# Optimization experiments

Measured on AMD Instinct MI355X. Metric: run time of the kernel, lower is better.

The kernel has to match this reference:

```python
import jax, jax.numpy as jnp
import numpy as np

NEG_INF = jnp.float32(-1e30)
EPS = 1e-7  # keras.backend.ctc_batch_cost epsilon


def ctc_batch_cost(y_true, y_pred):
    """Faithful CTC loss (keras ctc_batch_cost semantics): y_pred are
    probabilities [B,T,C], blank = C-1, full input/label lengths.
    Returns per-example negative log likelihood [B,1]."""
    B, T, C = y_pred.shape
    L = y_true.shape[1]
    S = 2 * L + 1  # extended label length (blanks interleaved)
    blank = C - 1

    log_probs = jnp.log(y_pred + EPS)  # [B,T,C]

    # Extended label sequence: blank, l0, blank, l1, ..., blank  -> [B,S]
    ext = jnp.full((B, S), blank, dtype=y_true.dtype)
    ext = ext.at[:, 1::2].set(y_true)

    # Skip transition allowed at s if ext[s] != blank and ext[s] != ext[s-2]
    skip = jnp.concatenate(
        [jnp.zeros((B, 2), dtype=bool),
         (ext[:, 2:] != blank) & (ext[:, 2:] != ext[:, :-2])], axis=1)  # [B,S]

    # Gather log-probs of extended labels per timestep: [T,B,S]
    lp_ext = jnp.take_along_axis(log_probs, ext[:, None, :], axis=2)  # [B,T,S]
    lp_ext = jnp.transpose(lp_ext, (1, 0, 2))  # [T,B,S]

    # alpha init at t=0: only positions 0 (blank) and 1 (first label)
    alpha0 = jnp.full((B, S), NEG_INF, dtype=log_probs.dtype)
    alpha0 = alpha0.at[:, 0].set(lp_ext[0, :, 0])
    alpha0 = alpha0.at[:, 1].set(lp_ext[0, :, 1])

    pad1 = jnp.full((B, 1), NEG_INF, dtype=log_probs.dtype)
    pad2 = jnp.full((B, 2), NEG_INF, dtype=log_probs.dtype)

    def step(alpha, lp_t):
        a_stay = alpha
        a_prev = jnp.concatenate([pad1, alpha[:, :-1]], axis=1)
        a_skip = jnp.where(skip, jnp.concatenate([pad2, alpha[:, :-2]], axis=1), NEG_INF)
        m = jnp.maximum(jnp.maximum(a_stay, a_prev), a_skip)
        lse = m + jnp.log(jnp.exp(a_stay - m) + jnp.exp(a_prev - m) + jnp.exp(a_skip - m))
        return lse + lp_t, None

    alpha_T, _ = jax.lax.scan(step, alpha0, lp_ext[1:])  # [B,S]

    # log P = logsumexp over last blank and last label positions
    end = jnp.stack([alpha_T[:, S - 1], alpha_T[:, S - 2]], axis=1)  # [B,2]
    loglik = jax.nn.logsumexp(end, axis=1)  # [B]
    return -loglik[:, None]  # [B,1] like keras ctc_batch_cost


def setup_inputs() -> dict:
    key = jax.random.key(0)
    k1, k2 = jax.random.split(key)
    B, T, C, L = 512, 512, 128, 32
    y_true = jax.random.randint(k1, (B, L), 0, C - 1, dtype=jnp.int64 if jax.config.read('jax_enable_x64') else jnp.int32)
    y_pred = jax.random.uniform(k2, (B, T, C), dtype=jnp.float32)
    return {"y_true": y_true, "y_pred": y_pred}


def reference(y_true, y_pred):
    return ctc_batch_cost(y_true, y_pred)
```

## Files before the change

### kernel.cpp

```cpp
#include <hip/hip_runtime.h>


#define EPSF 1e-7f

constexpr int T_  = 512;
constexpr int C_  = 128;
constexpr int L_  = 32;
constexpr int NG  = 127;
constexpr int PFG = 8;

__device__ __forceinline__ float wshr1(float x) {
    return __int_as_float(
        __builtin_amdgcn_mov_dpp(__float_as_int(x), 0x138, 0xf, 0xf, true));
}

__launch_bounds__(64)
__global__ void ctc_loss_kernel(const int* __restrict__ y_true,
                                const float* __restrict__ y_pred,
                                float* __restrict__ out) {
    const int b    = blockIdx.x;
    const int lane = threadIdx.x;

    const float* bb  = y_pred + (size_t)b * T_ * C_;
    const int*   lbl = y_true + b * L_;

    int   cls0;
    float sg0;
    {
        int c0 = C_ - 1;
        if (lane >= 1 && (lane & 1)) c0 = lbl[(lane - 1) >> 1];
        cls0 = c0;
        float s = 0.f;
        if (lane >= 3 && (lane & 1)) {
            const int c = lbl[(lane - 1) >> 1];
            if (c != lbl[((lane - 1) >> 1) - 1]) s = 1.f;
        }
        sg0 = s;
    }

    float a       = (lane < 2) ? (bb[cls0] + EPSF) : 0.f;
    float a64     = 0.f;
    int   e_total = 0;

    auto loadQ = [&](float (&Pk)[4], int g) {
        const float* r = bb + (size_t)(1 + 4 * g) * C_ + cls0;
        Pk[0] = r[0];
        Pk[1] = r[C_];
        Pk[2] = r[2 * C_];
        Pk[3] = r[3 * C_];
    };

    auto sample_eb = [&]() -> int {
        int mb = __builtin_amdgcn_readlane(__float_as_int(a), 3);
#pragma unroll
        for (int i = 1; i < 16; ++i) {
            const int v = __builtin_amdgcn_readlane(__float_as_int(a), 4 * i + 3);
            mb = (v > mb) ? v : mb;
        }
        const int eb = (int)((unsigned)mb >> 23);
        return (eb > 27) ? eb : 27;
    };

    auto apply_scale = [&](int eb) {
        e_total += eb - 127;
        const float inv = __uint_as_float((unsigned)(254 - eb) << 23);
        a   *= inv;
        a64 *= inv;
    };

    auto group4 = [&](const float (&P)[4]) {
        float x = a;
        float z = a64;
#pragma unroll
        for (int r = 0; r < 4; ++r) {
            const float q  = P[r] + EPSF;
            const float qs = wshr1(q);
            const float x1 = wshr1(x);
            const float x2 = wshr1(x1);
            z = (z + x) * qs;
            x = (x + x1 + sg0 * x2) * q;
        }
        a   = x;
        a64 = z;
    };

    float Q[PFG][4];
#pragma unroll
    for (int k = 0; k < PFG; ++k) loadQ(Q[k], k);

    int ebp = sample_eb();

    for (int g0 = 0; g0 < 112; g0 += PFG) {
#pragma unroll
        for (int k = 0; k < PFG; ++k) {
            group4(Q[k]);
            apply_scale(ebp);
            ebp = sample_eb();
            loadQ(Q[k], g0 + k + PFG);
        }
    }

#pragma unroll
    for (int k = 0; k < PFG; ++k) {
        group4(Q[k]);
        apply_scale(ebp);
        ebp = sample_eb();
        if (k < 7) loadQ(Q[k], 120 + k);
    }

    float qo[3];
#pragma unroll
    for (int r = 0; r < 3; ++r) qo[r] = bb[(size_t)(509 + r) * C_ + cls0];

#pragma unroll
    for (int k = 0; k < 7; ++k) {
        group4(Q[k]);
        apply_scale(ebp);
        if (k < 6) ebp = sample_eb();
    }

#pragma unroll
    for (int r = 0; r < 3; ++r) {
        const float p1 = wshr1(a);
        const float p2 = wshr1(p1);
        const float qb = wshr1(qo[r]);
        const float anew = (a + p1 + sg0 * p2) * (qo[r] + EPSF);
        a64 = (a64 + a) * (qb + EPSF);
        a = anew;
    }

    if (lane == 63) {
        out[b] = -(__logf(a + a64) + (float)e_total * 0.6931471805599453f);
    }
}

extern "C" void kernel_launch(void* const* d_in, const int* in_sizes, int n_in,
                              void* d_out, int out_size, void* d_ws, size_t ws_size,
                              hipStream_t stream) {
    const int*   y_true = (const int*)d_in[0];
    const float* y_pred = (const float*)d_in[1];
    float*       out    = (float*)d_out;

    const int B = out_size;
    ctc_loss_kernel<<<B, 64, 0, stream>>>(y_true, y_pred, out);
}
```

Before: 194.8 us.

## Split CTC recursion into forward and backward halves meeting at midpoint

Each block now runs two wavefronts: one computes the forward alpha recursion over the first half of time steps and the other a backward (beta) recursion over reversed time and labels on the second half. The halves are combined at the midpoint through shared memory with a double-precision dot product and wave reduction. This halves the serial dependency chain per example, which is the latency bottleneck. In exchange it doubles the threads per block and adds a sync, a shared-memory exchange and a double-precision reduction at the end.

```diff
diff --git a/kernel.cpp b/kernel.cpp
--- a/kernel.cpp
+++ b/kernel.cpp
@@ -6,7 +6,6 @@
 constexpr int T_  = 512;
 constexpr int C_  = 128;
 constexpr int L_  = 32;
-constexpr int NG  = 127;
 constexpr int PFG = 8;
 
 __device__ __forceinline__ float wshr1(float x) {
@@ -14,63 +13,65 @@
         __builtin_amdgcn_mov_dpp(__float_as_int(x), 0x138, 0xf, 0xf, true));
 }
 
-__launch_bounds__(64)
+__device__ __forceinline__ int sample_eb(float v) {
+    int mb = __builtin_amdgcn_readlane(__float_as_int(v), 3);
+#pragma unroll
+    for (int i = 1; i < 16; ++i) {
+        const int t = __builtin_amdgcn_readlane(__float_as_int(v), 4 * i + 3);
+        mb = (t > mb) ? t : mb;
+    }
+    const int eb = (int)((unsigned)mb >> 23);
+    return (eb > 27) ? eb : 27;
+}
+
+__launch_bounds__(128)
 __global__ void ctc_loss_kernel(const int* __restrict__ y_true,
                                 const float* __restrict__ y_pred,
                                 float* __restrict__ out) {
+    __shared__ float shR[65];
+    __shared__ int   shE;
+
     const int b    = blockIdx.x;
-    const int lane = threadIdx.x;
+    const int tid  = threadIdx.x;
+    const int lane = tid & 63;
+    const int w    = tid >> 6;
 
     const float* bb  = y_pred + (size_t)b * T_ * C_;
     const int*   lbl = y_true + b * L_;
 
-    int   cls0;
-    float sg0;
-    {
-        int c0 = C_ - 1;
-        if (lane >= 1 && (lane & 1)) c0 = lbl[(lane - 1) >> 1];
-        cls0 = c0;
-        float s = 0.f;
-        if (lane >= 3 && (lane & 1)) {
-            const int c = lbl[(lane - 1) >> 1];
-            if (c != lbl[((lane - 1) >> 1) - 1]) s = 1.f;
+    int   cls0 = C_ - 1;
+    float sg0  = 0.f;
+    if (w == 0) {
+        if (lane & 1) cls0 = lbl[(lane - 1) >> 1];
+        if ((lane & 1) && lane >= 3) {
+            const int li = (lane - 1) >> 1;
+            if (lbl[li] != lbl[li - 1]) sg0 = 1.f;
         }
-        sg0 = s;
+    } else {
+        if (lane & 1) cls0 = lbl[31 - ((lane - 1) >> 1)];
+        if ((lane & 1) && lane >= 3) {
+            const int li = (lane - 1) >> 1;
+            if (lbl[31 - li] != lbl[32 - li]) sg0 = 1.f;
+        }
     }
 
-    float a       = (lane < 2) ? (bb[cls0] + EPSF) : 0.f;
+    auto rowp = [&](int t) {
+        const int orig = w ? (511 - t) : t;
+        return bb + (size_t)orig * C_ + cls0;
+    };
+    const int rs = w ? -C_ : C_;
+
+    float a       = (lane < 2) ? (rowp(0)[0] + EPSF) : 0.f;
     float a64     = 0.f;
     int   e_total = 0;
 
     auto loadQ = [&](float (&Pk)[4], int g) {
-        const float* r = bb + (size_t)(1 + 4 * g) * C_ + cls0;
-        Pk[0] = r[0];
-        Pk[1] = r[C_];
-        Pk[2] = r[2 * C_];
-        Pk[3] = r[3 * C_];
-    };
-
-    auto sample_eb = [&]() -> int {
-        int mb = __builtin_amdgcn_readlane(__float_as_int(a), 3);
-#pragma unroll
-        for (int i = 1; i < 16; ++i) {
-            const int v = __builtin_amdgcn_readlane(__float_as_int(a), 4 * i + 3);
-            mb = (v > mb) ? v : mb;
-        }
-        const int eb = (int)((unsigned)mb >> 23);
-        return (eb > 27) ? eb : 27;
-    };
-
-    auto apply_scale = [&](int eb) {
-        e_total += eb - 127;
-        const float inv = __uint_as_float((unsigned)(254 - eb) << 23);
-        a   *= inv;
-        a64 *= inv;
+        const float* r = rowp(1 + 4 * g);
+        Pk[0] = r[0]; Pk[1] = r[rs]; Pk[2] = r[2 * rs]; Pk[3] = r[3 * rs];
     };
 
     auto group4 = [&](const float (&P)[4]) {
-        float x = a;
-        float z = a64;
+        float x = a, z = a64;
 #pragma unroll
         for (int r = 0; r < 4; ++r) {
             const float q  = P[r] + EPSF;
@@ -80,57 +81,74 @@
             z = (z + x) * qs;
             x = (x + x1 + sg0 * x2) * q;
         }
-        a   = x;
-        a64 = z;
+        a = x; a64 = z;
+    };
+
+    auto scale = [&](int eb) {
+        e_total += eb - 127;
+        const float inv = __uint_as_float((unsigned)(254 - eb) << 23);
+        a *= inv; a64 *= inv;
     };
 
     float Q[PFG][4];
 #pragma unroll
     for (int k = 0; k < PFG; ++k) loadQ(Q[k], k);
+    int ebp = sample_eb(a);
 
-    int ebp = sample_eb();
-
-    for (int g0 = 0; g0 < 112; g0 += PFG) {
+    for (int g0 = 0; g0 < 48; g0 += PFG) {
 #pragma unroll
         for (int k = 0; k < PFG; ++k) {
-            group4(Q[k]);
-            apply_scale(ebp);
-            ebp = sample_eb();
+            group4(Q[k]); scale(ebp); ebp = sample_eb(a);
             loadQ(Q[k], g0 + k + PFG);
         }
     }
-
 #pragma unroll
     for (int k = 0; k < PFG; ++k) {
-        group4(Q[k]);
-        apply_scale(ebp);
-        ebp = sample_eb();
-        if (k < 7) loadQ(Q[k], 120 + k);
+        group4(Q[k]); scale(ebp); ebp = sample_eb(a);
+        if (k < 7) loadQ(Q[k], 56 + k);
     }
-
     float qo[3];
 #pragma unroll
-    for (int r = 0; r < 3; ++r) qo[r] = bb[(size_t)(509 + r) * C_ + cls0];
-
+    for (int r = 0; r < 3; ++r) qo[r] = rowp(253 + r)[0];
 #pragma unroll
     for (int k = 0; k < 7; ++k) {
-        group4(Q[k]);
-        apply_scale(ebp);
-        if (k < 6) ebp = sample_eb();
+        group4(Q[k]); scale(ebp);
+        if (k < 6) ebp = sample_eb(a);
     }
-
 #pragma unroll
     for (int r = 0; r < 3; ++r) {
         const float p1 = wshr1(a);
         const float p2 = wshr1(p1);
         const float qb = wshr1(qo[r]);
-        const float anew = (a + p1 + sg0 * p2) * (qo[r] + EPSF);
+        const float an = (a + p1 + sg0 * p2) * (qo[r] + EPSF);
         a64 = (a64 + a) * (qb + EPSF);
-        a = anew;
+        a = an;
     }
 
-    if (lane == 63) {
-        out[b] = -(__logf(a + a64) + (float)e_total * 0.6931471805599453f);
+    if (w == 1) {
+        shR[lane] = a;
+        if (lane == 63) shR[64] = a64;
+        if (lane == 0)  shE = e_total;
+    }
+    __syncthreads();
+
+    if (w == 0) {
+        const float a1 = wshr1(a);
+        const float a2 = wshr1(a1);
+        const float abar = a + a1 + sg0 * a2;
+        double p = (double)abar * (double)shR[64 - lane];
+        if (lane == 63) p += (double)(a64 + a) * (double)shR[0];
+#pragma unroll
+        for (int m = 1; m < 64; m <<= 1) p += __shfl(p, lane ^ m);
+        if (lane == 0) {
+            if (p < 1e-300) p = 1e-300;
+            const unsigned long long bt = __double_as_longlong(p);
+            const int k = (int)((bt >> 52) & 0x7FFULL) - 1023;
+            const double mant = __longlong_as_double(
+                (bt & 0x000FFFFFFFFFFFFFULL) | 0x3FF0000000000000ULL);
+            out[b] = -(__logf((float)mant) +
+                       (float)(e_total + shE + k) * 0.6931471805599453f);
+        }
     }
 }
 
@@ -142,5 +160,5 @@
     float*       out    = (float*)d_out;
 
     const int B = out_size;
-    ctc_loss_kernel<<<B, 64, 0, stream>>>(y_true, y_pred, out);
+    ctc_loss_kernel<<<B, 128, 0, stream>>>(y_true, y_pred, out);
 }
```

After: 194.4 us. No clear change (-0.2%).
